# Performance work log

Hardware: AMD Instinct MI355X
Metric: run time of the kernel (lower is better)

Reference implementation:

```python
import jax, jax.numpy as jnp
import numpy as np
import math

B, S, D, H = 4, 1024, 1024, 16
DK = D // H  # 64


def setup_inputs() -> dict:
    key = jax.random.key(0)
    ks = jax.random.split(key, 16)
    inp = {
        "query": jax.random.normal(ks[0], (B, S, D), dtype=jnp.float32),
        "key": jax.random.normal(ks[1], (B, S, D), dtype=jnp.float32),
        "value": jax.random.normal(ks[2], (B, S, D), dtype=jnp.float32),
        "mask": jax.random.randint(ks[3], (B, 1, S, S), 0, 2, dtype=jnp.int32),
        "relation_bias_matrix": jax.random.normal(ks[4], (S, S, DK), dtype=jnp.float32),
    }
    # learned params: 3 input projections + output projection (nn.Linear d_model->d_model)
    sc = 1.0 / math.sqrt(D)
    for i, nm in enumerate(["Wq", "Wk", "Wv", "Wo"]):
        inp[nm] = jax.random.normal(ks[5 + i], (D, D), dtype=jnp.float32) * sc
    for i, nm in enumerate(["bq", "bk", "bv", "bo"]):
        inp[nm] = jax.random.normal(ks[9 + i], (D,), dtype=jnp.float32) * sc
    return inp


def reference(query, key, value, mask, relation_bias_matrix,
              Wq, bq, Wk, bk, Wv, bv, Wo, bo):
    b, s, d = query.shape
    h, dk = H, DK
    scale = 1.0 / math.sqrt(dk)

    def proj(x, W, bias):
        # [B,S,D] -> [B,H,S,dk]
        return (x @ W + bias).reshape(b, s, h, dk).transpose(0, 2, 1, 3)

    q = proj(query, Wq, bq)
    k = proj(key, Wk, bk)
    v = proj(value, Wv, bv)

    # NOTE: source scales score1 by 1/sqrt(dk), then scales (score1+score2) again.
    score1 = jnp.einsum('bhid,bhjd->bhij', q, k) * scale
    # relation bias: rel[i,j,:] is a d_k key for (query pos i, key pos j)
    score2 = jnp.einsum('bhid,ijd->bhij', q, relation_bias_matrix)
    scores = (score1 + score2) * scale
    scores = jnp.where(mask == 0, jnp.asarray(-1e9, scores.dtype), scores)
    p_attn = jax.nn.softmax(scores, axis=-1)  # dropout p=0.0 -> identity
    x = jnp.einsum('bhij,bhjd->bhid', p_attn, v)
    x = x.transpose(0, 2, 1, 3).reshape(b, s, d)
    return x @ Wo + bo
```

## Files before the change

kernel.cpp:

```cpp
#include <hip/hip_runtime.h>
#include <hip/hip_bf16.h>


typedef unsigned short u16;
typedef unsigned int u32;
typedef __attribute__((ext_vector_type(8))) short bf16x8;
typedef __attribute__((ext_vector_type(4))) float f32x4;

#define SB 1024
#define DM 1024
#define NHD 16
#define DKH 64
#define NBATCH 4

#define PIN() do { __builtin_amdgcn_sched_barrier(0); asm volatile("" ::: "memory"); } while (0)

__device__ __forceinline__ u16 f2bf(float x) {
  union { __hip_bfloat16 b; u16 u; } c;
  c.b = __float2bfloat16(x);
  return c.u;
}

__device__ __forceinline__ f32x4 mfma16(bf16x8 a, bf16x8 b, f32x4 c) {
  return __builtin_amdgcn_mfma_f32_16x16x32_bf16(a, b, c, 0, 0, 0);
}

__device__ __forceinline__ bf16x8 cvt8r(float4 v0, float4 v1) {
  bf16x8 r;
  r[0] = (short)f2bf(v0.x); r[1] = (short)f2bf(v0.y);
  r[2] = (short)f2bf(v0.z); r[3] = (short)f2bf(v0.w);
  r[4] = (short)f2bf(v1.x); r[5] = (short)f2bf(v1.y);
  r[6] = (short)f2bf(v1.z); r[7] = (short)f2bf(v1.w);
  return r;
}

__global__ void ra_convert_in(const float* __restrict__ q, const float* __restrict__ k,
                              const float* __restrict__ v,
                              u16* __restrict__ Xq, u16* __restrict__ Xk, u16* __restrict__ Xv)
{
  const int z = blockIdx.y;
  const float* src = (z == 0) ? q : (z == 1) ? k : v;
  u16* dst = (z == 0) ? Xq : (z == 1) ? Xk : Xv;
  const int n4 = NBATCH * SB * DM / 4;
  int idx = blockIdx.x * blockDim.x + threadIdx.x;
  int stride = gridDim.x * blockDim.x;
  for (int i = idx; i < n4; i += stride) {
    float4 v4 = *((const float4*)src + i);
    uint2 o;
    o.x = (u32)f2bf(v4.x) | ((u32)f2bf(v4.y) << 16);
    o.y = (u32)f2bf(v4.z) | ((u32)f2bf(v4.w) << 16);
    *((uint2*)dst + i) = o;
  }
}

__global__ void ra_transpose_w(const float* __restrict__ Wq, const float* __restrict__ Wk,
                               const float* __restrict__ Wv, const float* __restrict__ Wo,
                               u16* __restrict__ WqT, u16* __restrict__ WkT,
                               u16* __restrict__ WvT, u16* __restrict__ WoT)
{
  const int z = blockIdx.z;
  const float* W = (z == 0) ? Wq : (z == 1) ? Wk : (z == 2) ? Wv : Wo;
  u16* WT = (z == 0) ? WqT : (z == 1) ? WkT : (z == 2) ? WvT : WoT;
  __shared__ float tile[32][33];
  const int x0 = blockIdx.x * 32, y0 = blockIdx.y * 32;
  const int tx = threadIdx.x, ty = threadIdx.y;
#pragma unroll
  for (int yy = 0; yy < 4; ++yy) {
    int r = ty + yy * 8;
    tile[r][tx] = W[(size_t)(y0 + r) * DM + x0 + tx];
  }
  __syncthreads();
#pragma unroll
  for (int yy = 0; yy < 4; ++yy) {
    int r = ty + yy * 8;
    WT[(size_t)(x0 + r) * DM + y0 + tx] = f2bf(tile[tx][r]);
  }
}

__device__ __forceinline__ void gemm_core_128(const u16* __restrict__ A, const u16* __restrict__ Bt,
                                              int bm0, int bn0, u16* sh, f32x4 (&acc)[4][4])
{
  u16* As = sh;
  u16* Bs = sh + 128 * 72;
  const int tid = threadIdx.x;
  const int lane = tid & 63, wid = tid >> 6;
  const int l15 = lane & 15, l4 = lane >> 4;
  const int wr = (wid >> 1) * 64, wc = (wid & 1) * 64;
  for (int k0 = 0; k0 < DM; k0 += 64) {
#pragma unroll
    for (int it = 0; it < 4; ++it) {
      int c = tid + it * 256;
      int rw = c >> 3, kc = c & 7;
      *(uint4*)(As + rw * 72 + kc * 8) = *(const uint4*)(A + (size_t)(bm0 + rw) * DM + k0 + kc * 8);
      *(uint4*)(Bs + rw * 72 + kc * 8) = *(const uint4*)(Bt + (size_t)(bn0 + rw) * DM + k0 + kc * 8);
    }
    __syncthreads();
#pragma unroll
    for (int kf = 0; kf < 2; ++kf) {
      bf16x8 a[4], b[4];
#pragma unroll
      for (int mf = 0; mf < 4; ++mf)
        a[mf] = *(const bf16x8*)(As + (wr + mf * 16 + l15) * 72 + kf * 32 + l4 * 8);
#pragma unroll
      for (int nf = 0; nf < 4; ++nf)
        b[nf] = *(const bf16x8*)(Bs + (wc + nf * 16 + l15) * 72 + kf * 32 + l4 * 8);
#pragma unroll
      for (int mf = 0; mf < 4; ++mf)
#pragma unroll
        for (int nf = 0; nf < 4; ++nf)
          acc[mf][nf] = mfma16(a[mf], b[nf], acc[mf][nf]);
    }
    __syncthreads();
  }
}

__global__ __launch_bounds__(256, 2)
void ra_proj_gemm(const u16* __restrict__ Xq, const u16* __restrict__ Xk, const u16* __restrict__ Xv,
                  const u16* __restrict__ WqT, const u16* __restrict__ WkT, const u16* __restrict__ WvT,
                  const float* __restrict__ bq, const float* __restrict__ bk, const float* __restrict__ bv,
                  u16* __restrict__ q_ws, u16* __restrict__ k_ws, u16* __restrict__ vT_ws)
{
  __shared__ alignas(16) u16 sh[128 * 72 * 2];
  const int mode = blockIdx.z;
  const u16* A  = (mode == 0) ? Xq : (mode == 1) ? Xk : Xv;
  const u16* Bt = (mode == 0) ? WqT : (mode == 1) ? WkT : WvT;
  const float* bias = (mode == 0) ? bq : (mode == 1) ? bk : bv;
  const int bm0 = blockIdx.x * 128, bn0 = blockIdx.y * 128;
  f32x4 acc[4][4] = {};
  gemm_core_128(A, Bt, bm0, bn0, sh, acc);
  const int tid = threadIdx.x;
  const int lane = tid & 63, wid = tid >> 6;
  const int l15 = lane & 15, l4 = lane >> 4;
  const int wr = (wid >> 1) * 64, wc = (wid & 1) * 64;
  const int b_idx = bm0 >> 10;
  const int srow0 = bm0 & (SB - 1);
  if (mode < 2) {
    u16* outp = (mode == 0) ? q_ws : k_ws;
#pragma unroll
    for (int nf = 0; nf < 4; ++nf) {
      int nn = bn0 + wc + nf * 16 + l15;
      float bv_ = bias[nn];
      int h = nn >> 6, d = nn & 63;
#pragma unroll
      for (int mf = 0; mf < 4; ++mf)
#pragma unroll
        for (int r = 0; r < 4; ++r) {
          int m = wr + mf * 16 + l4 * 4 + r;
          outp[((size_t)(b_idx * NHD + h) * SB + srow0 + m) * DKH + d] = f2bf(acc[mf][nf][r] + bv_);
        }
    }
  } else {
    u16* ct = sh;
#pragma unroll
    for (int nf = 0; nf < 4; ++nf) {
      int nl = wc + nf * 16 + l15;
      float bv_ = bias[bn0 + nl];
#pragma unroll
      for (int mf = 0; mf < 4; ++mf)
#pragma unroll
        for (int r = 0; r < 4; ++r) {
          int m = wr + mf * 16 + l4 * 4 + r;
          ct[nl * 136 + m] = f2bf(acc[mf][nf][r] + bv_);
        }
    }
    __syncthreads();
#pragma unroll
    for (int it = 0; it < 8; ++it) {
      int c = tid + it * 256;
      int n = c >> 4, mc2 = c & 15;
      uint4 v = *(const uint4*)(ct + n * 136 + mc2 * 8);
      int nn = bn0 + n;
      int h = nn >> 6, d = nn & 63;
      *(uint4*)(vT_ws + ((size_t)(b_idx * NHD + h) * DKH + d) * SB + srow0 + mc2 * 8) = v;
    }
  }
}

__global__ __launch_bounds__(256, 2)
void ra_out_gemm(const u16* __restrict__ X, const u16* __restrict__ WoT,
                 const float* __restrict__ bo, float* __restrict__ out)
{
  __shared__ alignas(16) u16 sh[128 * 72 * 2];
  const int bm0 = blockIdx.x * 128, bn0 = blockIdx.y * 128;
  f32x4 acc[4][4] = {};
  gemm_core_128(X, WoT, bm0, bn0, sh, acc);
  const int tid = threadIdx.x;
  const int lane = tid & 63, wid = tid >> 6;
  const int l15 = lane & 15, l4 = lane >> 4;
  const int wr = (wid >> 1) * 64, wc = (wid & 1) * 64;
#pragma unroll
  for (int nf = 0; nf < 4; ++nf) {
    int nn = bn0 + wc + nf * 16 + l15;
    float bv_ = bo[nn];
#pragma unroll
    for (int mf = 0; mf < 4; ++mf)
#pragma unroll
      for (int r = 0; r < 4; ++r) {
        int m = wr + mf * 16 + l4 * 4 + r;
        out[(size_t)(bm0 + m) * DM + nn] = acc[mf][nf][r] + bv_;
      }
  }
}

__global__ __launch_bounds__(512, 1)
void ra_attn(const u16* __restrict__ q_ws, const u16* __restrict__ k_ws,
             const u16* __restrict__ vT_ws, const int* __restrict__ mask,
             const float* __restrict__ rel, u16* __restrict__ x_ws)
{
  __shared__ alignas(16) u16 Kb[2][16384];
  __shared__ alignas(16) u16 Vb[2][16416];
  __shared__ alignas(16) _Float16 s2t[2][5184];

  const int tid = threadIdx.x, wid = tid >> 6, lane = tid & 63;
  const int l15 = lane & 15, l4 = lane >> 4;
  const int g = blockIdx.y, i0 = blockIdx.x * 16, bh0 = g * NHD;
  const float scl1 = 0.125f, scl2 = 0.015625f;

  bf16x8 q1[2][2];
  bf16x8 q2[2][2];
#pragma unroll
  for (int bx = 0; bx < 2; ++bx) {
    const u16* qp = q_ws + ((size_t)(bh0 + wid * 2 + bx) * SB + i0 + l15) * DKH + l4 * 8;
    q1[bx][0] = *(const bf16x8*)qp;
    q1[bx][1] = *(const bf16x8*)(qp + 32);
  }
#pragma unroll
  for (int ix = 0; ix < 2; ++ix) {
    const u16* qp = q_ws + ((size_t)(bh0 + l15) * SB + i0 + wid * 2 + ix) * DKH + l4 * 8;
    q2[ix][0] = *(const bf16x8*)qp;
    q2[ix][1] = *(const bf16x8*)(qp + 32);
  }

#define STAGE_K(JB, BUF)                                                                  \
  {                                                                                       \
    _Pragma("unroll") for (int n = 0; n < 4; ++n) {                                       \
      const int C = n * 512 + wid * 64 + lane;                                            \
      const int bh_ = C >> 7, j_ = (C >> 3) & 15, c_ = C & 7;                             \
      const u16* gp = k_ws + ((size_t)(bh0 + bh_) * SB + (JB) + j_) * DKH + (c_ ^ (j_ & 7)) * 8; \
      u16* lp = Kb[BUF] + (n * 512 + wid * 64) * 8;                                       \
      __builtin_amdgcn_global_load_lds((const __attribute__((address_space(1))) unsigned int*)gp, \
                                       (__attribute__((address_space(3))) unsigned int*)lp, 16, 0, 0); \
    }                                                                                     \
  }
#define STAGE_V(JB, BUF)                                                                  \
  {                                                                                       \
    _Pragma("unroll") for (int n = 0; n < 4; ++n) {                                       \
      const int C = n * 512 + wid * 64 + lane;                                            \
      const int bh_ = C >> 7, d_ = (C >> 1) & 63, h_ = C & 1;                             \
      const u16* gp = vT_ws + ((size_t)(bh0 + bh_) * DKH + d_) * SB + (JB) + h_ * 8;      \
      u16* lp = Vb[BUF] + (n * 512 + wid * 64) * 8;                                       \
      __builtin_amdgcn_global_load_lds((const __attribute__((address_space(1))) unsigned int*)gp, \
                                       (__attribute__((address_space(3))) unsigned int*)lp, 16, 0, 0); \
    }                                                                                     \
  }

  float4 rr[2][4];
  int4 mr;
  STAGE_K(0, 0);
  STAGE_V(0, 0);
#pragma unroll
  for (int ix = 0; ix < 2; ++ix) {
    const float* rp = rel + ((size_t)(i0 + wid * 2 + ix) * SB + l15) * DKH + l4 * 8;
    rr[ix][0] = *(const float4*)rp;
    rr[ix][1] = *(const float4*)(rp + 4);
    rr[ix][2] = *(const float4*)(rp + 32);
    rr[ix][3] = *(const float4*)(rp + 36);
  }
  mr = *(const int4*)(mask + ((size_t)g * SB + i0 + l15) * SB + l4 * 4);
  PIN();
  __syncthreads();

  f32x4 acc_o[2][4] = {};
  float m_run[2] = {-1e30f, -1e30f}, l_run[2] = {0.f, 0.f};

  for (int jt = 0; jt < 64; ++jt) {
    const int jb = jt * 16;
    const int jbn = (jt < 63) ? jb + 16 : jb;
    const int cur = jt & 1, nxt = cur ^ 1;

    STAGE_K(jbn, nxt);
    PIN();

    f32x4 sc1[2];
#pragma unroll
    for (int bx = 0; bx < 2; ++bx) {
      f32x4 t = {};
#pragma unroll
      for (int kf = 0; kf < 2; ++kf) {
        bf16x8 ka = *(const bf16x8*)(Kb[cur] +
            ((((wid * 2 + bx) * 16 + l15) * 8 + ((kf * 4 + l4) ^ (l15 & 7))) * 8));
        t = mfma16(ka, q1[bx][kf], t);
      }
      sc1[bx] = t;
    }

#pragma unroll
    for (int ix = 0; ix < 2; ++ix) {
      const int i2 = wid * 2 + ix;
      bf16x8 rb0 = cvt8r(rr[ix][0], rr[ix][1]);
      bf16x8 rb1 = cvt8r(rr[ix][2], rr[ix][3]);
      f32x4 t = {};
      t = mfma16(q2[ix][0], rb0, t);
      t = mfma16(q2[ix][1], rb1, t);
      union { _Float16 h[4]; uint2 u; } w;
#pragma unroll
      for (int r = 0; r < 4; ++r) w.h[r] = (_Float16)(t[r] * scl1);
      *(uint2*)&s2t[cur][i2 * 324 + l15 * 20 + l4 * 4] = w.u;
    }

    __syncthreads();

    float s2f[2][4];
#pragma unroll
    for (int bx = 0; bx < 2; ++bx)
#pragma unroll
      for (int r = 0; r < 4; ++r)
        s2f[bx][r] = (float)s2t[cur][l15 * 324 + (l4 * 4 + r) * 20 + (wid * 2 + bx)];

#pragma unroll
    for (int ix = 0; ix < 2; ++ix) {
      const float* rp = rel + ((size_t)(i0 + wid * 2 + ix) * SB + jbn + l15) * DKH + l4 * 8;
      rr[ix][0] = *(const float4*)rp;
      rr[ix][1] = *(const float4*)(rp + 4);
      rr[ix][2] = *(const float4*)(rp + 32);
      rr[ix][3] = *(const float4*)(rp + 36);
    }
    STAGE_V(jbn, nxt);
    PIN();

    float fscs[2];
    bf16x8 pa[2];
#pragma unroll
    for (int bx = 0; bx < 2; ++bx) {
      float sv[4];
      sv[0] = (mr.x == 0) ? -1e9f : sc1[bx][0] * scl2 + s2f[bx][0];
      sv[1] = (mr.y == 0) ? -1e9f : sc1[bx][1] * scl2 + s2f[bx][1];
      sv[2] = (mr.z == 0) ? -1e9f : sc1[bx][2] * scl2 + s2f[bx][2];
      sv[3] = (mr.w == 0) ? -1e9f : sc1[bx][3] * scl2 + s2f[bx][3];
      float tmax = fmaxf(fmaxf(sv[0], sv[1]), fmaxf(sv[2], sv[3]));
      tmax = fmaxf(tmax, __shfl_xor(tmax, 16));
      tmax = fmaxf(tmax, __shfl_xor(tmax, 32));
      const float m_new = fmaxf(m_run[bx], tmax);
      const float fsc = __expf(m_run[bx] - m_new);
      float p0 = __expf(sv[0] - m_new), p1 = __expf(sv[1] - m_new);
      float p2 = __expf(sv[2] - m_new), p3 = __expf(sv[3] - m_new);
      float psum = p0 + p1 + p2 + p3;
      psum += __shfl_xor(psum, 16);
      psum += __shfl_xor(psum, 32);
      l_run[bx] = l_run[bx] * fsc + psum;
      m_run[bx] = m_new;
      fscs[bx] = fsc;
      union { bf16x8 v; u32 w[4]; } pk;
      pk.w[0] = (u32)f2bf(p0) | ((u32)f2bf(p1) << 16);
      pk.w[1] = (u32)f2bf(p2) | ((u32)f2bf(p3) << 16);
      pk.w[2] = 0; pk.w[3] = 0;
      pa[bx] = pk.v;
    }
    mr = *(const int4*)(mask + ((size_t)g * SB + i0 + l15) * SB + jbn + l4 * 4);
    PIN();

#pragma unroll
    for (int bx = 0; bx < 2; ++bx) {
      float f0 = __shfl(fscs[bx], l4 * 4 + 0);
      float f1 = __shfl(fscs[bx], l4 * 4 + 1);
      float f2 = __shfl(fscs[bx], l4 * 4 + 2);
      float f3 = __shfl(fscs[bx], l4 * 4 + 3);
#pragma unroll
      for (int df = 0; df < 4; ++df) {
        union { bf16x8 v; uint2 q[2]; } vb;
        vb.q[0] = *(const uint2*)(Vb[cur] +
                   (((wid * 2 + bx) * 64 + df * 16 + l15) * 16 + l4 * 4));
        vb.q[1] = make_uint2(0, 0);
        f32x4 c = acc_o[bx][df];
        c[0] *= f0; c[1] *= f1; c[2] *= f2; c[3] *= f3;
        acc_o[bx][df] = mfma16(pa[bx], vb.v, c);
      }
    }
  }

#pragma unroll
  for (int bx = 0; bx < 2; ++bx) {
    float inv0 = 1.f / __shfl(l_run[bx], l4 * 4 + 0);
    float inv1 = 1.f / __shfl(l_run[bx], l4 * 4 + 1);
    float inv2 = 1.f / __shfl(l_run[bx], l4 * 4 + 2);
    float inv3 = 1.f / __shfl(l_run[bx], l4 * 4 + 3);
    const int col0 = (wid * 2 + bx) * DKH;
#pragma unroll
    for (int df = 0; df < 4; ++df) {
      const int col = col0 + df * 16 + l15;
      x_ws[((size_t)g * SB + i0 + l4 * 4 + 0) * DM + col] = f2bf(acc_o[bx][df][0] * inv0);
      x_ws[((size_t)g * SB + i0 + l4 * 4 + 1) * DM + col] = f2bf(acc_o[bx][df][1] * inv1);
      x_ws[((size_t)g * SB + i0 + l4 * 4 + 2) * DM + col] = f2bf(acc_o[bx][df][2] * inv2);
      x_ws[((size_t)g * SB + i0 + l4 * 4 + 3) * DM + col] = f2bf(acc_o[bx][df][3] * inv3);
    }
  }
#undef STAGE_K
#undef STAGE_V
}

extern "C" void kernel_launch(void* const* d_in, const int* in_sizes, int n_in,
                              void* d_out, int out_size, void* d_ws, size_t ws_size,
                              hipStream_t stream) {
  const float* query = (const float*)d_in[0];
  const float* key_  = (const float*)d_in[1];
  const float* value = (const float*)d_in[2];
  const int*   mask  = (const int*)d_in[3];
  const float* rel   = (const float*)d_in[4];
  const float* Wq = (const float*)d_in[5];
  const float* Wk = (const float*)d_in[6];
  const float* Wv = (const float*)d_in[7];
  const float* Wo = (const float*)d_in[8];
  const float* bq = (const float*)d_in[9];
  const float* bk = (const float*)d_in[10];
  const float* bv = (const float*)d_in[11];
  const float* bo = (const float*)d_in[12];
  float* out = (float*)d_out;
  char* ws = (char*)d_ws;

  u16* Xq   = (u16*)(ws + (0ull));
  u16* Xk   = (u16*)(ws + (8ull << 20));
  u16* Xv   = (u16*)(ws + (16ull << 20));
  u16* WqT  = (u16*)(ws + (24ull << 20));
  u16* WkT  = (u16*)(ws + (26ull << 20));
  u16* WvT  = (u16*)(ws + (28ull << 20));
  u16* WoT  = (u16*)(ws + (30ull << 20));
  u16* q_ws = (u16*)(ws + (32ull << 20));
  u16* k_ws = (u16*)(ws + (40ull << 20));
  u16* vT_ws= (u16*)(ws + (48ull << 20));
  u16* x_ws = (u16*)(ws + (56ull << 20));

  ra_convert_in<<<dim3(1024, 3), 256, 0, stream>>>(query, key_, value, Xq, Xk, Xv);
  ra_transpose_w<<<dim3(32, 32, 4), dim3(32, 8), 0, stream>>>(Wq, Wk, Wv, Wo, WqT, WkT, WvT, WoT);
  ra_proj_gemm<<<dim3(32, 8, 3), 256, 0, stream>>>(Xq, Xk, Xv, WqT, WkT, WvT, bq, bk, bv,
                                                   q_ws, k_ws, vT_ws);
  ra_attn<<<dim3(64, 4), 512, 0, stream>>>(q_ws, k_ws, vT_ws, mask, rel, x_ws);
  ra_out_gemm<<<dim3(32, 8), 256, 0, stream>>>(x_ws, WoT, bo, out);
}
```

Measured before the change: 372.5 us.

## Restructure attention to one wave per head with register-prefetched K/V and bitpacked mask

The attention kernel now launches 1024 threads, so each of 16 waves owns one head, and the LDS staging of K and V is dropped. K, V and rel tiles are prefetched straight into registers, and the MFMA operand roles are swapped so rows map cleanly without per-row shuffles. A new pre-pass packs the int32 mask into bits, which cuts the mask traffic inside the attention loop. The cost is an extra kernel launch, bit-mask storage placed in the reused Xv workspace region, and the loss of cross-wave K/V sharing through LDS.

```diff
diff --git a/kernel.cpp b/kernel.cpp
--- a/kernel.cpp
+++ b/kernel.cpp
@@ -4,6 +4,7 @@
 
 typedef unsigned short u16;
 typedef unsigned int u32;
+typedef unsigned long long u64;
 typedef __attribute__((ext_vector_type(8))) short bf16x8;
 typedef __attribute__((ext_vector_type(4))) float f32x4;
 
@@ -202,200 +203,150 @@
   }
 }
 
-__global__ __launch_bounds__(512, 1)
+__global__ __launch_bounds__(256)
+void ra_mask_pack(const int* __restrict__ mask, u32* __restrict__ mb)
+{
+  const size_t t = (size_t)blockIdx.x * 256 + threadIdx.x;
+  const int lane = threadIdx.x & 63;
+  u64 b = __ballot(mask[t] != 0);
+  if (lane == 0) *(u64*)(mb + (t >> 6) * 2) = b;
+}
+
+__global__ __launch_bounds__(1024, 1)
 void ra_attn(const u16* __restrict__ q_ws, const u16* __restrict__ k_ws,
-             const u16* __restrict__ vT_ws, const int* __restrict__ mask,
+             const u16* __restrict__ vT_ws, const u32* __restrict__ mb,
              const float* __restrict__ rel, u16* __restrict__ x_ws)
 {
-  __shared__ alignas(16) u16 Kb[2][16384];
-  __shared__ alignas(16) u16 Vb[2][16416];
-  __shared__ alignas(16) _Float16 s2t[2][5184];
+  __shared__ _Float16 s2t[2][16 * 292 + 8];
 
   const int tid = threadIdx.x, wid = tid >> 6, lane = tid & 63;
   const int l15 = lane & 15, l4 = lane >> 4;
-  const int g = blockIdx.y, i0 = blockIdx.x * 16, bh0 = g * NHD;
+  const int g = blockIdx.y, i0 = blockIdx.x * 16;
+  const int bh_g = g * NHD + wid;
   const float scl1 = 0.125f, scl2 = 0.015625f;
 
-  bf16x8 q1[2][2];
-  bf16x8 q2[2][2];
-#pragma unroll
-  for (int bx = 0; bx < 2; ++bx) {
-    const u16* qp = q_ws + ((size_t)(bh0 + wid * 2 + bx) * SB + i0 + l15) * DKH + l4 * 8;
-    q1[bx][0] = *(const bf16x8*)qp;
-    q1[bx][1] = *(const bf16x8*)(qp + 32);
-  }
-#pragma unroll
-  for (int ix = 0; ix < 2; ++ix) {
-    const u16* qp = q_ws + ((size_t)(bh0 + l15) * SB + i0 + wid * 2 + ix) * DKH + l4 * 8;
-    q2[ix][0] = *(const bf16x8*)qp;
-    q2[ix][1] = *(const bf16x8*)(qp + 32);
-  }
-
-#define STAGE_K(JB, BUF)                                                                  \
-  {                                                                                       \
-    _Pragma("unroll") for (int n = 0; n < 4; ++n) {                                       \
-      const int C = n * 512 + wid * 64 + lane;                                            \
-      const int bh_ = C >> 7, j_ = (C >> 3) & 15, c_ = C & 7;                             \
-      const u16* gp = k_ws + ((size_t)(bh0 + bh_) * SB + (JB) + j_) * DKH + (c_ ^ (j_ & 7)) * 8; \
-      u16* lp = Kb[BUF] + (n * 512 + wid * 64) * 8;                                       \
-      __builtin_amdgcn_global_load_lds((const __attribute__((address_space(1))) unsigned int*)gp, \
-                                       (__attribute__((address_space(3))) unsigned int*)lp, 16, 0, 0); \
-    }                                                                                     \
-  }
-#define STAGE_V(JB, BUF)                                                                  \
-  {                                                                                       \
-    _Pragma("unroll") for (int n = 0; n < 4; ++n) {                                       \
-      const int C = n * 512 + wid * 64 + lane;                                            \
-      const int bh_ = C >> 7, d_ = (C >> 1) & 63, h_ = C & 1;                             \
-      const u16* gp = vT_ws + ((size_t)(bh0 + bh_) * DKH + d_) * SB + (JB) + h_ * 8;      \
-      u16* lp = Vb[BUF] + (n * 512 + wid * 64) * 8;                                       \
-      __builtin_amdgcn_global_load_lds((const __attribute__((address_space(1))) unsigned int*)gp, \
-                                       (__attribute__((address_space(3))) unsigned int*)lp, 16, 0, 0); \
-    }                                                                                     \
-  }
-
-  float4 rr[2][4];
-  int4 mr;
-  STAGE_K(0, 0);
-  STAGE_V(0, 0);
-#pragma unroll
-  for (int ix = 0; ix < 2; ++ix) {
-    const float* rp = rel + ((size_t)(i0 + wid * 2 + ix) * SB + l15) * DKH + l4 * 8;
-    rr[ix][0] = *(const float4*)rp;
-    rr[ix][1] = *(const float4*)(rp + 4);
-    rr[ix][2] = *(const float4*)(rp + 32);
-    rr[ix][3] = *(const float4*)(rp + 36);
-  }
-  mr = *(const int4*)(mask + ((size_t)g * SB + i0 + l15) * SB + l4 * 4);
+  bf16x8 q1[2], q2[2];
+#pragma unroll
+  for (int kf = 0; kf < 2; ++kf) {
+    q1[kf] = *(const bf16x8*)(q_ws + ((size_t)bh_g * SB + i0 + l15) * DKH + kf * 32 + l4 * 8);
+    q2[kf] = *(const bf16x8*)(q_ws + ((size_t)(g * NHD + l15) * SB + i0 + wid) * DKH + kf * 32 + l4 * 8);
+  }
+
+  bf16x8 ka[2];
+  float4 rr[4];
+  uint2  vb2[4];
+  u32    mw;
+
+  const u16* kbase = k_ws + (size_t)bh_g * SB * DKH;
+  const u16* vbase = vT_ws + (size_t)bh_g * DKH * SB;
+  const float* rbase = rel + (size_t)(i0 + wid) * SB * DKH;
+  const u32* mbase = mb + ((size_t)g * SB + i0 + l15) * 32;
+
+#pragma unroll
+  for (int kf = 0; kf < 2; ++kf)
+    ka[kf] = *(const bf16x8*)(kbase + (size_t)l15 * DKH + kf * 32 + l4 * 8);
+  {
+    const float* rp = rbase + (size_t)l15 * DKH + l4 * 8;
+    rr[0] = *(const float4*)rp;       rr[1] = *(const float4*)(rp + 4);
+    rr[2] = *(const float4*)(rp + 32); rr[3] = *(const float4*)(rp + 36);
+  }
+#pragma unroll
+  for (int df = 0; df < 4; ++df)
+    vb2[df] = *(const uint2*)(vbase + (size_t)(df * 16 + l15) * SB + l4 * 4);
+  mw = mbase[0];
   PIN();
-  __syncthreads();
-
-  f32x4 acc_o[2][4] = {};
-  float m_run[2] = {-1e30f, -1e30f}, l_run[2] = {0.f, 0.f};
+
+  f32x4 acc_o[4] = {};
+  float m_run = -1e30f, l_run = 0.f;
 
   for (int jt = 0; jt < 64; ++jt) {
     const int jb = jt * 16;
     const int jbn = (jt < 63) ? jb + 16 : jb;
-    const int cur = jt & 1, nxt = cur ^ 1;
-
-    STAGE_K(jbn, nxt);
+    const int cur = jt & 1;
+
+    {
+      bf16x8 rb0 = cvt8r(rr[0], rr[1]);
+      bf16x8 rb1 = cvt8r(rr[2], rr[3]);
+      f32x4 t = {};
+      t = mfma16(rb0, q2[0], t);
+      t = mfma16(rb1, q2[1], t);
+      union { _Float16 h[4]; uint2 u; } w;
+#pragma unroll
+      for (int r = 0; r < 4; ++r) w.h[r] = (_Float16)(t[r] * scl1);
+      *(uint2*)&s2t[cur][wid * 292 + l15 * 18 + l4 * 4] = w.u;
+    }
+    {
+      const float* rp = rbase + (size_t)(jbn + l15) * DKH + l4 * 8;
+      rr[0] = *(const float4*)rp;       rr[1] = *(const float4*)(rp + 4);
+      rr[2] = *(const float4*)(rp + 32); rr[3] = *(const float4*)(rp + 36);
+    }
     PIN();
 
-    f32x4 sc1[2];
-#pragma unroll
-    for (int bx = 0; bx < 2; ++bx) {
-      f32x4 t = {};
-#pragma unroll
-      for (int kf = 0; kf < 2; ++kf) {
-        bf16x8 ka = *(const bf16x8*)(Kb[cur] +
-            ((((wid * 2 + bx) * 16 + l15) * 8 + ((kf * 4 + l4) ^ (l15 & 7))) * 8));
-        t = mfma16(ka, q1[bx][kf], t);
+    f32x4 sc1 = {};
+    sc1 = mfma16(ka[0], q1[0], sc1);
+    sc1 = mfma16(ka[1], q1[1], sc1);
+#pragma unroll
+    for (int kf = 0; kf < 2; ++kf)
+      ka[kf] = *(const bf16x8*)(kbase + (size_t)(jbn + l15) * DKH + kf * 32 + l4 * 8);
+    PIN();
+
+    __syncthreads();
+
+    float fsc;
+    bf16x8 pa;
+    {
+      uint2 s2u = *(const uint2*)&s2t[cur][l15 * 292 + wid * 18 + l4 * 4];
+      union { uint2 u; _Float16 h[4]; } s2c; s2c.u = s2u;
+      const int mbit = (jt & 1) * 16 + l4 * 4;
+      float sv[4];
+#pragma unroll
+      for (int r = 0; r < 4; ++r) {
+        float v = sc1[r] * scl2 + (float)s2c.h[r];
+        sv[r] = ((mw >> (mbit + r)) & 1u) ? v : -1e9f;
       }
-      sc1[bx] = t;
-    }
-
-#pragma unroll
-    for (int ix = 0; ix < 2; ++ix) {
-      const int i2 = wid * 2 + ix;
-      bf16x8 rb0 = cvt8r(rr[ix][0], rr[ix][1]);
-      bf16x8 rb1 = cvt8r(rr[ix][2], rr[ix][3]);
-      f32x4 t = {};
-      t = mfma16(q2[ix][0], rb0, t);
-      t = mfma16(q2[ix][1], rb1, t);
-      union { _Float16 h[4]; uint2 u; } w;
-#pragma unroll
-      for (int r = 0; r < 4; ++r) w.h[r] = (_Float16)(t[r] * scl1);
-      *(uint2*)&s2t[cur][i2 * 324 + l15 * 20 + l4 * 4] = w.u;
-    }
-
-    __syncthreads();
-
-    float s2f[2][4];
-#pragma unroll
-    for (int bx = 0; bx < 2; ++bx)
-#pragma unroll
-      for (int r = 0; r < 4; ++r)
-        s2f[bx][r] = (float)s2t[cur][l15 * 324 + (l4 * 4 + r) * 20 + (wid * 2 + bx)];
-
-#pragma unroll
-    for (int ix = 0; ix < 2; ++ix) {
-      const float* rp = rel + ((size_t)(i0 + wid * 2 + ix) * SB + jbn + l15) * DKH + l4 * 8;
-      rr[ix][0] = *(const float4*)rp;
-      rr[ix][1] = *(const float4*)(rp + 4);
-      rr[ix][2] = *(const float4*)(rp + 32);
-      rr[ix][3] = *(const float4*)(rp + 36);
-    }
-    STAGE_V(jbn, nxt);
-    PIN();
-
-    float fscs[2];
-    bf16x8 pa[2];
-#pragma unroll
-    for (int bx = 0; bx < 2; ++bx) {
-      float sv[4];
-      sv[0] = (mr.x == 0) ? -1e9f : sc1[bx][0] * scl2 + s2f[bx][0];
-      sv[1] = (mr.y == 0) ? -1e9f : sc1[bx][1] * scl2 + s2f[bx][1];
-      sv[2] = (mr.z == 0) ? -1e9f : sc1[bx][2] * scl2 + s2f[bx][2];
-      sv[3] = (mr.w == 0) ? -1e9f : sc1[bx][3] * scl2 + s2f[bx][3];
       float tmax = fmaxf(fmaxf(sv[0], sv[1]), fmaxf(sv[2], sv[3]));
       tmax = fmaxf(tmax, __shfl_xor(tmax, 16));
       tmax = fmaxf(tmax, __shfl_xor(tmax, 32));
-      const float m_new = fmaxf(m_run[bx], tmax);
-      const float fsc = __expf(m_run[bx] - m_new);
+      const float m_new = fmaxf(m_run, tmax);
+      fsc = __expf(m_run - m_new);
       float p0 = __expf(sv[0] - m_new), p1 = __expf(sv[1] - m_new);
       float p2 = __expf(sv[2] - m_new), p3 = __expf(sv[3] - m_new);
       float psum = p0 + p1 + p2 + p3;
       psum += __shfl_xor(psum, 16);
       psum += __shfl_xor(psum, 32);
-      l_run[bx] = l_run[bx] * fsc + psum;
-      m_run[bx] = m_new;
-      fscs[bx] = fsc;
+      l_run = l_run * fsc + psum;
+      m_run = m_new;
       union { bf16x8 v; u32 w[4]; } pk;
       pk.w[0] = (u32)f2bf(p0) | ((u32)f2bf(p1) << 16);
       pk.w[1] = (u32)f2bf(p2) | ((u32)f2bf(p3) << 16);
       pk.w[2] = 0; pk.w[3] = 0;
-      pa[bx] = pk.v;
-    }
-    mr = *(const int4*)(mask + ((size_t)g * SB + i0 + l15) * SB + jbn + l4 * 4);
+      pa = pk.v;
+    }
+
+#pragma unroll
+    for (int df = 0; df < 4; ++df) {
+      union { bf16x8 v; uint2 q[2]; } vv;
+      vv.q[0] = vb2[df];
+      vv.q[1] = make_uint2(0, 0);
+      f32x4 c = acc_o[df];
+      c[0] *= fsc; c[1] *= fsc; c[2] *= fsc; c[3] *= fsc;
+      acc_o[df] = mfma16(vv.v, pa, c);
+    }
+#pragma unroll
+    for (int df = 0; df < 4; ++df)
+      vb2[df] = *(const uint2*)(vbase + (size_t)(df * 16 + l15) * SB + jbn + l4 * 4);
+    mw = mbase[(jt + 1 < 64) ? ((jt + 1) >> 1) : 31];
     PIN();
-
-#pragma unroll
-    for (int bx = 0; bx < 2; ++bx) {
-      float f0 = __shfl(fscs[bx], l4 * 4 + 0);
-      float f1 = __shfl(fscs[bx], l4 * 4 + 1);
-      float f2 = __shfl(fscs[bx], l4 * 4 + 2);
-      float f3 = __shfl(fscs[bx], l4 * 4 + 3);
-#pragma unroll
-      for (int df = 0; df < 4; ++df) {
-        union { bf16x8 v; uint2 q[2]; } vb;
-        vb.q[0] = *(const uint2*)(Vb[cur] +
-                   (((wid * 2 + bx) * 64 + df * 16 + l15) * 16 + l4 * 4));
-        vb.q[1] = make_uint2(0, 0);
-        f32x4 c = acc_o[bx][df];
-        c[0] *= f0; c[1] *= f1; c[2] *= f2; c[3] *= f3;
-        acc_o[bx][df] = mfma16(pa[bx], vb.v, c);
-      }
-    }
-  }
-
-#pragma unroll
-  for (int bx = 0; bx < 2; ++bx) {
-    float inv0 = 1.f / __shfl(l_run[bx], l4 * 4 + 0);
-    float inv1 = 1.f / __shfl(l_run[bx], l4 * 4 + 1);
-    float inv2 = 1.f / __shfl(l_run[bx], l4 * 4 + 2);
-    float inv3 = 1.f / __shfl(l_run[bx], l4 * 4 + 3);
-    const int col0 = (wid * 2 + bx) * DKH;
-#pragma unroll
-    for (int df = 0; df < 4; ++df) {
-      const int col = col0 + df * 16 + l15;
-      x_ws[((size_t)g * SB + i0 + l4 * 4 + 0) * DM + col] = f2bf(acc_o[bx][df][0] * inv0);
-      x_ws[((size_t)g * SB + i0 + l4 * 4 + 1) * DM + col] = f2bf(acc_o[bx][df][1] * inv1);
-      x_ws[((size_t)g * SB + i0 + l4 * 4 + 2) * DM + col] = f2bf(acc_o[bx][df][2] * inv2);
-      x_ws[((size_t)g * SB + i0 + l4 * 4 + 3) * DM + col] = f2bf(acc_o[bx][df][3] * inv3);
-    }
-  }
-#undef STAGE_K
-#undef STAGE_V
+  }
+
+  const float inv = 1.f / l_run;
+#pragma unroll
+  for (int df = 0; df < 4; ++df) {
+    union { u16 h[4]; uint2 u; } o;
+#pragma unroll
+    for (int r = 0; r < 4; ++r) o.h[r] = f2bf(acc_o[df][r] * inv);
+    *(uint2*)(x_ws + ((size_t)g * SB + i0 + l15) * DM + wid * DKH + df * 16 + l4 * 4) = o.u;
+  }
 }
 
 extern "C" void kernel_launch(void* const* d_in, const int* in_sizes, int n_in,
@@ -428,11 +379,13 @@
   u16* k_ws = (u16*)(ws + (40ull << 20));
   u16* vT_ws= (u16*)(ws + (48ull << 20));
   u16* x_ws = (u16*)(ws + (56ull << 20));
+  u32* mb   = (u32*)(ws + (16ull << 20));
 
   ra_convert_in<<<dim3(1024, 3), 256, 0, stream>>>(query, key_, value, Xq, Xk, Xv);
   ra_transpose_w<<<dim3(32, 32, 4), dim3(32, 8), 0, stream>>>(Wq, Wk, Wv, Wo, WqT, WkT, WvT, WoT);
   ra_proj_gemm<<<dim3(32, 8, 3), 256, 0, stream>>>(Xq, Xk, Xv, WqT, WkT, WvT, bq, bk, bv,
                                                    q_ws, k_ws, vT_ws);
-  ra_attn<<<dim3(64, 4), 512, 0, stream>>>(q_ws, k_ws, vT_ws, mask, rel, x_ws);
+  ra_mask_pack<<<16384, 256, 0, stream>>>(mask, mb);
+  ra_attn<<<dim3(64, 4), 1024, 0, stream>>>(q_ws, k_ws, vT_ws, mb, rel, x_ws);
   ra_out_gemm<<<dim3(32, 8), 256, 0, stream>>>(x_ws, WoT, bo, out);
 }
```

Result: slower. 422.5 us (+13.4%).
